# Performance work log

Hardware: AMD Instinct MI355X
Metric: run time of the kernel (lower is better)

The kernel has to match this reference:

```python
import jax, jax.numpy as jnp
import numpy as np

OBS_LEN = 8
B = 262144
H = 16   # lstm hidden / MADE hidden / cond dim
D = 2    # trajectory input dim / flow dim
N_FLOWS = 4
CLAMP = 5.0


def _masks():
    # MADE masks for num_inputs=2, num_hidden=16 (ikostrikov get_mask)
    in_deg = jnp.arange(D) % D                      # [0, 1]
    hid_deg = jnp.zeros((H,), jnp.float32)          # arange(16) % (2-1) == 0
    out_deg = (jnp.arange(2 * D) % D - 1).astype(jnp.float32)  # [-1,0,-1,0]
    input_mask = (hid_deg[:, None] >= in_deg[None, :].astype(jnp.float32)).astype(jnp.float32)  # [16,2]
    hidden_mask = jnp.ones((H, H), jnp.float32)     # all degrees 0 -> full
    output_mask = (out_deg[:, None] >= hid_deg[None, :]).astype(jnp.float32)  # [4,16]
    return input_mask, hidden_mask, output_mask


def _made_ma(x, cond, p, masks):
    # x: [B,2], cond: [B,16] -> m, a: [B,2]
    im, hm, om = masks
    jW, jb, cW, hW, hb, oW, ob = p
    h = x @ (jW * im).T + jb + cond @ cW.T      # joiner (masked) + cond linear (no bias)
    h = jax.nn.relu(h)
    h = jax.nn.relu(h @ (hW * hm).T + hb)       # trunk hidden masked linear
    out = h @ (oW * om).T + ob                  # trunk output masked linear -> [B,4]
    m, a = out[:, :D], out[:, D:]
    a = CLAMP * jnp.tanh(a / CLAMP)             # soft log-scale clamp (clamp_flow)
    return m, a


def _made_inverse(u, cond, p, masks):
    x = jnp.zeros_like(u)
    for i in range(D):
        m, a = _made_ma(x, cond, p, masks)
        x = x.at[:, i].set(u[:, i] * jnp.exp(a[:, i]) + m[:, i])
    return x


def _maf_sample(noise, cond, made_params, masks):
    # modules = [MADE0,Rev,MADE1,Rev,MADE2,Rev,MADE3,Rev]; sample runs inverse in reversed order
    x = noise
    for k in reversed(range(N_FLOWS)):
        x = x[:, ::-1]                           # Reverse(2) inverse == flip
        p = tuple(t[k] for t in made_params)
        x = _made_inverse(x, cond, p, masks)
    return x


def _encode(traj, enc_W, enc_b, W_ih, W_hh, b_ih, b_hh, h0, c0):
    # obs_len LSTM loop; dropout is identity in eval/test mode
    def step(carry, x_t):
        h, c = carry
        e = jax.nn.relu(x_t @ enc_W.T + enc_b)                 # [B,16]
        g = e @ W_ih.T + b_ih + h @ W_hh.T + b_hh              # [B,64]
        i, f, gg, o = jnp.split(g, 4, axis=-1)                 # torch LSTMCell gate order
        c = jax.nn.sigmoid(f) * c + jax.nn.sigmoid(i) * jnp.tanh(gg)
        h = jax.nn.sigmoid(o) * jnp.tanh(c)
        return (h, c), None
    (h, c), _ = jax.lax.scan(step, (h0, c0), traj)
    return h


def setup_inputs() -> dict:
    key = jax.random.key(0)
    ks = jax.random.split(key, 16)
    s = 0.1
    return {
        "traj_rel": jax.random.normal(ks[0], (OBS_LEN + 1, B, D), jnp.float32),
        "obs_traj_pos": jax.random.normal(ks[1], (OBS_LEN, B, D), jnp.float32),
        "h0": jax.random.normal(ks[2], (B, H), jnp.float32),
        "c0": jax.random.normal(ks[3], (B, H), jnp.float32),
        "noise": jax.random.normal(ks[4], (B, D), jnp.float32),
        "enc_W": jax.random.normal(ks[5], (H, D), jnp.float32) * 0.2,
        "enc_b": jnp.zeros((H,), jnp.float32),
        "lstm_W_ih": jax.random.normal(ks[6], (4 * H, H), jnp.float32) * s,
        "lstm_W_hh": jax.random.normal(ks[7], (4 * H, H), jnp.float32) * 0.001,
        "lstm_b_ih": jnp.zeros((4 * H,), jnp.float32).at[H:2 * H].set(1.0),
        "lstm_b_hh": jnp.zeros((4 * H,), jnp.float32),
        "made_joiner_W": jax.random.normal(ks[8], (N_FLOWS, H, D), jnp.float32) * s,
        "made_joiner_b": jnp.zeros((N_FLOWS, H), jnp.float32),
        "made_cond_W": jax.random.normal(ks[9], (N_FLOWS, H, H), jnp.float32) * s,
        "made_hid_W": jax.random.normal(ks[10], (N_FLOWS, H, H), jnp.float32) * s,
        "made_hid_b": jnp.zeros((N_FLOWS, H), jnp.float32),
        "made_out_W": jax.random.normal(ks[11], (N_FLOWS, 2 * D, H), jnp.float32) * s,
        "made_out_b": jnp.zeros((N_FLOWS, 2 * D), jnp.float32),
    }


def reference(traj_rel, obs_traj_pos, h0, c0, noise,
              enc_W, enc_b, lstm_W_ih, lstm_W_hh, lstm_b_ih, lstm_b_hh,
              made_joiner_W, made_joiner_b, made_cond_W,
              made_hid_W, made_hid_b, made_out_W, made_out_b):
    masks = _masks()
    h = _encode(traj_rel[:OBS_LEN], enc_W, enc_b,
                lstm_W_ih, lstm_W_hh, lstm_b_ih, lstm_b_hh, h0, c0)  # [B,16]
    made_params = (made_joiner_W, made_joiner_b, made_cond_W,
                   made_hid_W, made_hid_b, made_out_W, made_out_b)
    goal = _maf_sample(noise, h, made_params, masks)                  # [B,2]
    return goal + obs_traj_pos[-1]                                    # mode='test' output_pred
```

## Files before the change

kernel.cpp:

```cpp
#include <hip/hip_runtime.h>

#define B_N 262144
#define OBS_N 8

typedef __attribute__((ext_vector_type(4))) _Float16 f16x4;
typedef __attribute__((ext_vector_type(2))) __fp16 fp16x2;
typedef __attribute__((ext_vector_type(4))) float f32x4;

#define LOG2E 1.44269504088896340736f

__device__ __forceinline__ float rcpf_(float x){ return __builtin_amdgcn_rcpf(x); }
__device__ __forceinline__ float exp2f_(float x){ return __builtin_amdgcn_exp2f(x); }
__device__ __forceinline__ float tanh_(float x){ return fmaf(-2.0f, rcpf_(exp2f_((2.0f*LOG2E) * x) + 1.0f), 1.0f); }

__device__ __forceinline__ f16x4 pack4(float a, float b, float c, float d){
    fp16x2 lo = __builtin_amdgcn_cvt_pkrtz(a, b);
    fp16x2 hi = __builtin_amdgcn_cvt_pkrtz(c, d);
    f16x4 r;
    r[0] = (_Float16)lo[0]; r[1] = (_Float16)lo[1];
    r[2] = (_Float16)hi[0]; r[3] = (_Float16)hi[1];
    return r;
}

#define MFMA16(a, b, c) __builtin_amdgcn_mfma_f32_16x16x16f16((a), (b), (c), 0, 0, 0)

__global__ __launch_bounds__(256, 5) void goal_kernel(
    const float* __restrict__ traj,
    const float* __restrict__ obsp,
    const float* __restrict__ h0,
    const float* __restrict__ c0,
    const float* __restrict__ noise,
    const float* __restrict__ encW,
    const float* __restrict__ encb,
    const float* __restrict__ Wih,
    const float* __restrict__ Whh,
    const float* __restrict__ bih,
    const float* __restrict__ bhh,
    const float* __restrict__ jW,
    const float* __restrict__ jb,
    const float* __restrict__ cW,
    const float* __restrict__ hW,
    const float* __restrict__ hb,
    const float* __restrict__ oW,
    const float* __restrict__ ob,
    float* __restrict__ out)
{
    const int lane = threadIdx.x & 63;
    const int wv   = threadIdx.x >> 6;
    const int q    = lane >> 4;
    const int s    = lane & 15;
    const int j4   = q * 4;
    const int col  = (blockIdx.x * 4 + wv) * 16 + s;

    f16x4 ew0h, ew1h, ebh;
    #pragma unroll
    for (int r = 0; r < 4; ++r) {
        ew0h[r] = (_Float16)encW[(j4 + r) * 2 + 0];
        ew1h[r] = (_Float16)encW[(j4 + r) * 2 + 1];
        ebh[r]  = (_Float16)encb[j4 + r];
    }

    const float gsc[4] = { -LOG2E, -LOG2E, -2.0f*LOG2E, -LOG2E };

    f16x4 wihA[4], whhA[4];
    f32x4 bias[4];
    #pragma unroll
    for (int m = 0; m < 4; ++m) {
        float4 wa = *(const float4*)(Wih + (16 * m + s) * 16 + j4);
        float4 wb = *(const float4*)(Whh + (16 * m + s) * 16 + j4);
        wihA[m] = pack4(wa.x*gsc[m], wa.y*gsc[m], wa.z*gsc[m], wa.w*gsc[m]);
        whhA[m] = pack4(wb.x*gsc[m], wb.y*gsc[m], wb.z*gsc[m], wb.w*gsc[m]);
        float4 b1 = *(const float4*)(bih + 16 * m + j4);
        float4 b2 = *(const float4*)(bhh + 16 * m + j4);
        f32x4 bv;
        bv[0] = (b1.x+b2.x)*gsc[m]; bv[1] = (b1.y+b2.y)*gsc[m];
        bv[2] = (b1.z+b2.z)*gsc[m]; bv[3] = (b1.w+b2.w)*gsc[m];
        bias[m] = bv;
    }

    f32x4 c_ = *(const f32x4*)(c0 + col * 16 + j4);
    float4 hv0 = *(const float4*)(h0 + col * 16 + j4);
    f16x4 hA = pack4(hv0.x, hv0.y, hv0.z, hv0.w);

    float2 nz = *(const float2*)(noise + col * 2);

    const float NEG2L2E = -2.0f * LOG2E;

    float2 xv = *(const float2*)(traj + col * 2);

    #pragma unroll 1
    for (int t = 0; t < OBS_N; ++t) {
        float2 nx;
        if (t < OBS_N - 1)
            nx = *(const float2*)(traj + (t + 1) * (B_N * 2) + col * 2);

        _Float16 hx = (_Float16)xv.x, hy = (_Float16)xv.y;
        f16x4 xx = { hx, hx, hx, hx };
        f16x4 yy = { hy, hy, hy, hy };
        f16x4 ef = ew0h * xx + ew1h * yy + ebh;
        #pragma unroll
        for (int r = 0; r < 4; ++r)
            ef[r] = ef[r] > (_Float16)0 ? ef[r] : (_Float16)0;

        f32x4 g[4];
        #pragma unroll
        for (int m = 0; m < 4; ++m) {
            g[m] = MFMA16(wihA[m], ef, bias[m]);
            g[m] = MFMA16(whhA[m], hA, g[m]);
        }

        float hn[4];
        #pragma unroll
        for (int r = 0; r < 4; ++r) {
            float Ei = exp2f_(g[0][r]);
            float Ef = exp2f_(g[1][r]);
            float Eg = exp2f_(g[2][r]);
            float Eo = exp2f_(g[3][r]);
            float pi = 1.0f + Ei, pg = 1.0f + Eg, pf = 1.0f + Ef;
            float m_ = pi * pg;
            float R1 = rcpf_(m_ * pf);
            float tt = fmaf(-Eg, pf, pf);
            float cn = fmaf(c_[r], m_, tt) * R1;
            c_[r] = cn;
            float Ec = exp2f_(NEG2L2E * cn);
            float R2 = rcpf_((1.0f + Ec) * (1.0f + Eo));
            hn[r] = fmaf(-Ec, R2, R2);
        }
        hA = pack4(hn[0], hn[1], hn[2], hn[3]);

        if (t < OBS_N - 1) xv = nx;
    }

    float x0 = nz.x, x1 = nz.y;

    #pragma unroll 1
    for (int kf = 3; kf >= 0; --kf) {
        float tsw = x0; x0 = x1; x1 = tsw;

        float ob0 = ob[kf*4 + 0], ob1 = ob[kf*4 + 1];
        float ob2 = ob[kf*4 + 2], ob3 = ob[kf*4 + 3] * 0.2f;
        float ea0 = exp2f_(7.2134752044f * tanh_(ob2 * 0.2f));
        x0 = fmaf(x0, ea0, ob0);

        float4 cw = *(const float4*)(cW + kf * 256 + s * 16 + j4);
        f16x4 cwA = pack4(cw.x, cw.y, cw.z, cw.w);
        float4 hw = *(const float4*)(hW + kf * 256 + s * 16 + j4);
        f16x4 hwA = pack4(hw.x, hw.y, hw.z, hw.w);
        float osc = ((s & 3) == 3) ? 0.2f : 1.0f;
        float4 ow = *(const float4*)(oW + kf * 64 + (s & 3) * 16 + j4);
        f16x4 owA = pack4(ow.x * osc, ow.y * osc, ow.z * osc, ow.w * osc);

        f32x4 a1;
        #pragma unroll
        for (int r = 0; r < 4; ++r)
            a1[r] = fmaf(jW[kf * 32 + (j4 + r) * 2], x0, jb[kf * 16 + j4 + r]);
        a1 = MFMA16(cwA, hA, a1);
        f16x4 h1 = pack4(fmaxf(a1[0],0.f), fmaxf(a1[1],0.f), fmaxf(a1[2],0.f), fmaxf(a1[3],0.f));

        f32x4 a2;
        #pragma unroll
        for (int r = 0; r < 4; ++r) a2[r] = hb[kf * 16 + j4 + r];
        a2 = MFMA16(hwA, h1, a2);
        f16x4 h2 = pack4(fmaxf(a2[0],0.f), fmaxf(a2[1],0.f), fmaxf(a2[2],0.f), fmaxf(a2[3],0.f));

        f32x4 a3;
        a3[0] = ob0; a3[1] = ob1; a3[2] = ob2; a3[3] = ob3;
        a3 = MFMA16(owA, h2, a3);

        x1 = fmaf(x1, exp2f_(7.2134752044f * tanh_(a3[3])), a3[1]);
    }

    if (q == 0) {
        float2 pp = *(const float2*)(obsp + (OBS_N - 1) * (B_N * 2) + col * 2);
        float2 o; o.x = x0 + pp.x; o.y = x1 + pp.y;
        *(float2*)(out + col * 2) = o;
    }
}

extern "C" void kernel_launch(void* const* d_in, const int* in_sizes, int n_in,
                              void* d_out, int out_size, void* d_ws, size_t ws_size,
                              hipStream_t stream) {
    goal_kernel<<<B_N / 64, 256, 0, stream>>>(
        (const float*)d_in[0],  (const float*)d_in[1],  (const float*)d_in[2],
        (const float*)d_in[3],  (const float*)d_in[4],  (const float*)d_in[5],
        (const float*)d_in[6],  (const float*)d_in[7],  (const float*)d_in[8],
        (const float*)d_in[9],  (const float*)d_in[10], (const float*)d_in[11],
        (const float*)d_in[12], (const float*)d_in[13], (const float*)d_in[14],
        (const float*)d_in[15], (const float*)d_in[16], (const float*)d_in[17],
        (float*)d_out);
}
```

Baseline: 49.87 us.

## Process four 16-column tiles per wave to amortize weight setup and interleave MFMAs

Each wave now handles 64 batch columns (four independent 16-wide tiles) instead of 16. The per-wave weight loading and packing for the LSTM and MADE layers is shared across all four tiles, and the grid shrinks by a factor of four. The independent tiles give the scheduler more MFMA and transcendental work to interleave, hiding latency. The flow's first-dimension exp-scale is also hoisted into a small precomputed table. The cost is higher register pressure, so launch bounds drop from 5 to 4 waves, which may reduce occupancy.

```diff
diff --git a/kernel.cpp b/kernel.cpp
--- a/kernel.cpp
+++ b/kernel.cpp
@@ -24,7 +24,7 @@
 
 #define MFMA16(a, b, c) __builtin_amdgcn_mfma_f32_16x16x16f16((a), (b), (c), 0, 0, 0)
 
-__global__ __launch_bounds__(256, 5) void goal_kernel(
+__global__ __launch_bounds__(256, 4) void goal_kernel(
     const float* __restrict__ traj,
     const float* __restrict__ obsp,
     const float* __restrict__ h0,
@@ -50,7 +50,11 @@
     const int q    = lane >> 4;
     const int s    = lane & 15;
     const int j4   = q * 4;
-    const int col  = (blockIdx.x * 4 + wv) * 16 + s;
+    const int base = blockIdx.x * 256 + wv * 64;
+
+    int col[4];
+    #pragma unroll
+    for (int i = 0; i < 4; ++i) col[i] = base + i * 16 + s;
 
     f16x4 ew0h, ew1h, ebh;
     #pragma unroll
@@ -78,69 +82,93 @@
         bias[m] = bv;
     }
 
-    f32x4 c_ = *(const f32x4*)(c0 + col * 16 + j4);
-    float4 hv0 = *(const float4*)(h0 + col * 16 + j4);
-    f16x4 hA = pack4(hv0.x, hv0.y, hv0.z, hv0.w);
-
-    float2 nz = *(const float2*)(noise + col * 2);
+    float ea0c[4];
+    #pragma unroll
+    for (int kf = 0; kf < 4; ++kf)
+        ea0c[kf] = exp2f_(7.2134752044f * tanh_(ob[kf*4 + 2] * 0.2f));
+
+    f32x4 c_[4];
+    f16x4 h_[4];
+    float2 xv[4];
+    #pragma unroll
+    for (int i = 0; i < 4; ++i) {
+        c_[i] = *(const f32x4*)(c0 + col[i] * 16 + j4);
+        float4 hv = *(const float4*)(h0 + col[i] * 16 + j4);
+        h_[i] = pack4(hv.x, hv.y, hv.z, hv.w);
+        xv[i] = *(const float2*)(traj + col[i] * 2);
+    }
 
     const float NEG2L2E = -2.0f * LOG2E;
-
-    float2 xv = *(const float2*)(traj + col * 2);
 
     #pragma unroll 1
     for (int t = 0; t < OBS_N; ++t) {
-        float2 nx;
-        if (t < OBS_N - 1)
-            nx = *(const float2*)(traj + (t + 1) * (B_N * 2) + col * 2);
-
-        _Float16 hx = (_Float16)xv.x, hy = (_Float16)xv.y;
-        f16x4 xx = { hx, hx, hx, hx };
-        f16x4 yy = { hy, hy, hy, hy };
-        f16x4 ef = ew0h * xx + ew1h * yy + ebh;
-        #pragma unroll
-        for (int r = 0; r < 4; ++r)
-            ef[r] = ef[r] > (_Float16)0 ? ef[r] : (_Float16)0;
-
-        f32x4 g[4];
-        #pragma unroll
-        for (int m = 0; m < 4; ++m) {
-            g[m] = MFMA16(wihA[m], ef, bias[m]);
-            g[m] = MFMA16(whhA[m], hA, g[m]);
-        }
-
-        float hn[4];
-        #pragma unroll
-        for (int r = 0; r < 4; ++r) {
-            float Ei = exp2f_(g[0][r]);
-            float Ef = exp2f_(g[1][r]);
-            float Eg = exp2f_(g[2][r]);
-            float Eo = exp2f_(g[3][r]);
-            float pi = 1.0f + Ei, pg = 1.0f + Eg, pf = 1.0f + Ef;
-            float m_ = pi * pg;
-            float R1 = rcpf_(m_ * pf);
-            float tt = fmaf(-Eg, pf, pf);
-            float cn = fmaf(c_[r], m_, tt) * R1;
-            c_[r] = cn;
-            float Ec = exp2f_(NEG2L2E * cn);
-            float R2 = rcpf_((1.0f + Ec) * (1.0f + Eo));
-            hn[r] = fmaf(-Ec, R2, R2);
-        }
-        hA = pack4(hn[0], hn[1], hn[2], hn[3]);
-
-        if (t < OBS_N - 1) xv = nx;
-    }
-
-    float x0 = nz.x, x1 = nz.y;
+        float2 nx[4];
+        if (t < OBS_N - 1) {
+            #pragma unroll
+            for (int i = 0; i < 4; ++i)
+                nx[i] = *(const float2*)(traj + (t + 1) * (B_N * 2) + col[i] * 2);
+        }
+
+        #pragma unroll
+        for (int i = 0; i < 4; ++i) {
+            _Float16 hx = (_Float16)xv[i].x, hy = (_Float16)xv[i].y;
+            f16x4 xx = { hx, hx, hx, hx };
+            f16x4 yy = { hy, hy, hy, hy };
+            f16x4 ef = ew0h * xx + ew1h * yy + ebh;
+            #pragma unroll
+            for (int r = 0; r < 4; ++r)
+                ef[r] = ef[r] > (_Float16)0 ? ef[r] : (_Float16)0;
+
+            f32x4 g[4];
+            #pragma unroll
+            for (int m = 0; m < 4; ++m) {
+                g[m] = MFMA16(wihA[m], ef, bias[m]);
+                g[m] = MFMA16(whhA[m], h_[i], g[m]);
+            }
+
+            float hn[4];
+            #pragma unroll
+            for (int r = 0; r < 4; ++r) {
+                float Ei = exp2f_(g[0][r]);
+                float Ef = exp2f_(g[1][r]);
+                float Eg = exp2f_(g[2][r]);
+                float Eo = exp2f_(g[3][r]);
+                float pi = 1.0f + Ei, pg = 1.0f + Eg, pf = 1.0f + Ef;
+                float m_ = pi * pg;
+                float R1 = rcpf_(m_ * pf);
+                float cn = fmaf(c_[i][r], m_, fmaf(-Eg, pf, pf)) * R1;
+                c_[i][r] = cn;
+                float Ec = exp2f_(NEG2L2E * cn);
+                float R2 = rcpf_((1.0f + Ec) * (1.0f + Eo));
+                hn[r] = fmaf(-Ec, R2, R2);
+            }
+            h_[i] = pack4(hn[0], hn[1], hn[2], hn[3]);
+        }
+
+        if (t < OBS_N - 1) {
+            #pragma unroll
+            for (int i = 0; i < 4; ++i) xv[i] = nx[i];
+        }
+    }
+
+    float x0[4], x1[4];
+    #pragma unroll
+    for (int i = 0; i < 4; ++i) {
+        float2 nz = *(const float2*)(noise + col[i] * 2);
+        x0[i] = nz.x; x1[i] = nz.y;
+    }
 
     #pragma unroll 1
     for (int kf = 3; kf >= 0; --kf) {
-        float tsw = x0; x0 = x1; x1 = tsw;
-
-        float ob0 = ob[kf*4 + 0], ob1 = ob[kf*4 + 1];
-        float ob2 = ob[kf*4 + 2], ob3 = ob[kf*4 + 3] * 0.2f;
-        float ea0 = exp2f_(7.2134752044f * tanh_(ob2 * 0.2f));
-        x0 = fmaf(x0, ea0, ob0);
+        #pragma unroll
+        for (int i = 0; i < 4; ++i) {
+            float tsw = x0[i]; x0[i] = x1[i]; x1[i] = tsw;
+        }
+
+        float4 ob4 = *(const float4*)(ob + kf * 4);
+        #pragma unroll
+        for (int i = 0; i < 4; ++i)
+            x0[i] = fmaf(x0[i], ea0c[kf], ob4.x);
 
         float4 cw = *(const float4*)(cW + kf * 256 + s * 16 + j4);
         f16x4 cwA = pack4(cw.x, cw.y, cw.z, cw.w);
@@ -149,38 +177,53 @@
         float osc = ((s & 3) == 3) ? 0.2f : 1.0f;
         float4 ow = *(const float4*)(oW + kf * 64 + (s & 3) * 16 + j4);
         f16x4 owA = pack4(ow.x * osc, ow.y * osc, ow.z * osc, ow.w * osc);
-
-        f32x4 a1;
-        #pragma unroll
-        for (int r = 0; r < 4; ++r)
-            a1[r] = fmaf(jW[kf * 32 + (j4 + r) * 2], x0, jb[kf * 16 + j4 + r]);
-        a1 = MFMA16(cwA, hA, a1);
-        f16x4 h1 = pack4(fmaxf(a1[0],0.f), fmaxf(a1[1],0.f), fmaxf(a1[2],0.f), fmaxf(a1[3],0.f));
-
-        f32x4 a2;
-        #pragma unroll
-        for (int r = 0; r < 4; ++r) a2[r] = hb[kf * 16 + j4 + r];
-        a2 = MFMA16(hwA, h1, a2);
-        f16x4 h2 = pack4(fmaxf(a2[0],0.f), fmaxf(a2[1],0.f), fmaxf(a2[2],0.f), fmaxf(a2[3],0.f));
-
-        f32x4 a3;
-        a3[0] = ob0; a3[1] = ob1; a3[2] = ob2; a3[3] = ob3;
-        a3 = MFMA16(owA, h2, a3);
-
-        x1 = fmaf(x1, exp2f_(7.2134752044f * tanh_(a3[3])), a3[1]);
+        float4 jwa = *(const float4*)(jW + kf * 32 + j4 * 2);
+        float4 jwb = *(const float4*)(jW + kf * 32 + j4 * 2 + 4);
+        float4 jb4 = *(const float4*)(jb + kf * 16 + j4);
+        float4 hb4 = *(const float4*)(hb + kf * 16 + j4);
+
+        f16x4 h1[4];
+        #pragma unroll
+        for (int i = 0; i < 4; ++i) {
+            f32x4 a1;
+            a1[0] = fmaf(jwa.x, x0[i], jb4.x);
+            a1[1] = fmaf(jwa.z, x0[i], jb4.y);
+            a1[2] = fmaf(jwb.x, x0[i], jb4.z);
+            a1[3] = fmaf(jwb.z, x0[i], jb4.w);
+            a1 = MFMA16(cwA, h_[i], a1);
+            h1[i] = pack4(fmaxf(a1[0],0.f), fmaxf(a1[1],0.f), fmaxf(a1[2],0.f), fmaxf(a1[3],0.f));
+        }
+        f16x4 h2[4];
+        #pragma unroll
+        for (int i = 0; i < 4; ++i) {
+            f32x4 a2;
+            a2[0] = hb4.x; a2[1] = hb4.y; a2[2] = hb4.z; a2[3] = hb4.w;
+            a2 = MFMA16(hwA, h1[i], a2);
+            h2[i] = pack4(fmaxf(a2[0],0.f), fmaxf(a2[1],0.f), fmaxf(a2[2],0.f), fmaxf(a2[3],0.f));
+        }
+        #pragma unroll
+        for (int i = 0; i < 4; ++i) {
+            f32x4 a3;
+            a3[0] = 0.f; a3[1] = ob4.y; a3[2] = 0.f; a3[3] = ob4.w * 0.2f;
+            a3 = MFMA16(owA, h2[i], a3);
+            x1[i] = fmaf(x1[i], exp2f_(7.2134752044f * tanh_(a3[3])), a3[1]);
+        }
     }
 
     if (q == 0) {
-        float2 pp = *(const float2*)(obsp + (OBS_N - 1) * (B_N * 2) + col * 2);
-        float2 o; o.x = x0 + pp.x; o.y = x1 + pp.y;
-        *(float2*)(out + col * 2) = o;
+        #pragma unroll
+        for (int i = 0; i < 4; ++i) {
+            float2 pp = *(const float2*)(obsp + (OBS_N - 1) * (B_N * 2) + col[i] * 2);
+            float2 o; o.x = x0[i] + pp.x; o.y = x1[i] + pp.y;
+            *(float2*)(out + col[i] * 2) = o;
+        }
     }
 }
 
 extern "C" void kernel_launch(void* const* d_in, const int* in_sizes, int n_in,
                               void* d_out, int out_size, void* d_ws, size_t ws_size,
                               hipStream_t stream) {
-    goal_kernel<<<B_N / 64, 256, 0, stream>>>(
+    goal_kernel<<<B_N / 256, 256, 0, stream>>>(
         (const float*)d_in[0],  (const float*)d_in[1],  (const float*)d_in[2],
         (const float*)d_in[3],  (const float*)d_in[4],  (const float*)d_in[5],
         (const float*)d_in[6],  (const float*)d_in[7],  (const float*)d_in[8],
```

Result: slower. 69.74 us (+39.8%).
